# Performance work log

Measured on AMD Instinct MI355X. Metric: run time of the kernel, lower is better.

The kernel has to match this reference:

```python
import jax, jax.numpy as jnp
import numpy as np

B, S, D = 2, 2048, 2048
HQ, HK, HD = 16, 8, 128          # query heads, kv heads, head_dim
EPS = 1e-6
ROPE_THETA = 10000.0
SCALE = HD ** -0.5


def setup_inputs() -> dict:
    key = jax.random.key(0)
    ks = jax.random.split(key, 6)
    s = lambda fan_in: 1.0 / np.sqrt(fan_in)
    return {
        "hidden_states": jax.random.normal(ks[0], (B, S, D), jnp.float32),
        "positions": jnp.arange(S, dtype=jnp.int32),
        "Wq": jax.random.normal(ks[1], (D, HQ * HD), jnp.float32) * s(D),
        "Wk": jax.random.normal(ks[2], (D, HK * HD), jnp.float32) * s(D),
        "Wv": jax.random.normal(ks[3], (D, HK * HD), jnp.float32) * s(D),
        "Wo": jax.random.normal(ks[4], (HQ * HD, D), jnp.float32) * s(HQ * HD),
        "q_norm_w": jnp.ones((HD,), jnp.float32),
        "k_norm_w": jnp.ones((HD,), jnp.float32),
    }


def _rmsnorm(x, w):
    # RMSNorm over last (head_dim) axis, as in q_norm/k_norm
    var = jnp.mean(jnp.square(x), axis=-1, keepdims=True)
    return x * jax.lax.rsqrt(var + EPS) * w


def _rope(x, positions):
    # x: [B, S, H, HD]; rotate_half-style RoPE (Qwen3 convention)
    half = HD // 2
    inv_freq = 1.0 / (ROPE_THETA ** (jnp.arange(0, half, dtype=jnp.float32) / half))
    angles = positions.astype(jnp.float32)[:, None] * inv_freq[None, :]  # [S, half]
    cos = jnp.cos(angles)[None, :, None, :]  # [1, S, 1, half]
    sin = jnp.sin(angles)[None, :, None, :]
    x1, x2 = x[..., :half], x[..., half:]
    return jnp.concatenate([x1 * cos - x2 * sin, x2 * cos + x1 * sin], axis=-1)


def reference(hidden_states, positions, Wq, Wk, Wv, Wo, q_norm_w, k_norm_w):
    b, s, _ = hidden_states.shape
    q = (hidden_states @ Wq).reshape(b, s, HQ, HD)
    k = (hidden_states @ Wk).reshape(b, s, HK, HD)
    v = (hidden_states @ Wv).reshape(b, s, HK, HD)

    q = _rmsnorm(q, q_norm_w)
    k = _rmsnorm(k, k_norm_w)

    q = _rope(q, positions)
    k = _rope(k, positions)

    # GQA: repeat KV heads to match query heads
    groups = HQ // HK
    k = jnp.repeat(k, groups, axis=2)  # [B, S, HQ, HD]
    v = jnp.repeat(v, groups, axis=2)

    scores = jnp.einsum("bqhd,bkhd->bhqk", q, k) * SCALE  # [B, HQ, S, S]
    causal = jnp.tril(jnp.ones((s, s), dtype=bool))
    scores = jnp.where(causal[None, None], scores, jnp.float32(-jnp.inf))
    attn = jax.nn.softmax(scores, axis=-1)

    out = jnp.einsum("bhqk,bkhd->bqhd", attn, v).reshape(b, s, HQ * HD)
    return out @ Wo
```

## Files before the change

kernel.cpp:

```cpp
#include <hip/hip_runtime.h>
#include <cstdint>
#include <cstddef>

typedef _Float16 half8 __attribute__((ext_vector_type(8)));
typedef _Float16 half4 __attribute__((ext_vector_type(4)));
typedef float f32x4 __attribute__((ext_vector_type(4)));

#define DI __device__ __forceinline__

DI void gld_lds16(void* sp, const void* gp) {
  __builtin_amdgcn_global_load_lds(
      (const __attribute__((address_space(1))) void*)gp,
      (__attribute__((address_space(3))) void*)sp, 16, 0, 0);
}

template <int N>
DI void vmwait() { asm volatile("s_waitcnt vmcnt(%0)" :: "n"(N) : "memory"); }

DI void barrier_raw() {
  asm volatile("" ::: "memory");
  __builtin_amdgcn_s_barrier();
  asm volatile("" ::: "memory");
}

__global__ __launch_bounds__(256) void prep(const float* __restrict__ hs,
                                            const float* __restrict__ Wq,
                                            const float* __restrict__ Wk,
                                            const float* __restrict__ Wv,
                                            const float* __restrict__ Wo,
                                            _Float16* __restrict__ Xh,
                                            _Float16* __restrict__ Wqkvt,
                                            _Float16* __restrict__ Wot) {
  const int bid = blockIdx.x;
  if (bid >= 12288) {
    const int i = (bid - 12288) * 256 + threadIdx.x;
    const float4* p = (const float4*)hs + (size_t)i * 2;
    const float4 a = p[0], b = p[1];
    half8 h;
    h[0] = (_Float16)a.x; h[1] = (_Float16)a.y; h[2] = (_Float16)a.z; h[3] = (_Float16)a.w;
    h[4] = (_Float16)b.x; h[5] = (_Float16)b.y; h[6] = (_Float16)b.z; h[7] = (_Float16)b.w;
    *(half8*)(Xh + (size_t)i * 8) = h;
    return;
  }
  const float* in;
  _Float16* outp;
  int C, t;
  if (bid < 4096)      { in = Wq; outp = Wqkvt;                        C = 2048; t = bid; }
  else if (bid < 6144) { in = Wk; outp = Wqkvt + (size_t)2048 * 2048;  C = 1024; t = bid - 4096; }
  else if (bid < 8192) { in = Wv; outp = Wqkvt + (size_t)3072 * 2048;  C = 1024; t = bid - 6144; }
  else                 { in = Wo; outp = Wot;                          C = 2048; t = bid - 8192; }
  __shared__ float tl[32][33];
  const int tx = threadIdx.x & 31, ty = threadIdx.x >> 5;
  const int ctiles = C >> 5;
  const int tc = t % ctiles, tr = t / ctiles;
  const int r0 = tr * 32, c0 = tc * 32;
#pragma unroll
  for (int i = 0; i < 4; i++)
    tl[ty + 8 * i][tx] = in[(size_t)(r0 + ty + 8 * i) * C + c0 + tx];
  __syncthreads();
#pragma unroll
  for (int i = 0; i < 4; i++) {
    const int rr = ty + 8 * i;
    outp[(size_t)(c0 + rr) * 2048 + r0 + tx] = (_Float16)tl[tx][rr];
  }
}

#define QPHASE(Q, STAGE, VMW)                                                  \
  {                                                                            \
    half8 afr[2][2];                                                           \
    _Pragma("unroll") for (int j = 0; j < 2; j++)                              \
      _Pragma("unroll") for (int ks = 0; ks < 2; ks++) {                       \
        const int arow = wm * 128 + ((Q) * 2 + j) * 16 + lo;                   \
        afr[j][ks] =                                                           \
            *(const half8*)&sA[sa][arow * 64 + (((ks * 4 + hi) ^ lo7) << 3)];  \
      }                                                                        \
    STAGE;                                                                     \
    VMW;                                                                       \
    barrier_raw();                                                             \
    asm volatile("s_waitcnt lgkmcnt(0)" ::: "memory");                         \
    __builtin_amdgcn_sched_barrier(0);                                         \
    __builtin_amdgcn_s_setprio(1);                                             \
    _Pragma("unroll") for (int j = 0; j < 2; j++)                              \
      _Pragma("unroll") for (int nf = 0; nf < 4; nf++)                         \
        _Pragma("unroll") for (int ks = 0; ks < 2; ks++)                       \
          acc[(Q) * 2 + j][nf] = __builtin_amdgcn_mfma_f32_16x16x32_f16(       \
              afr[j][ks], bfr[nf][ks], acc[(Q) * 2 + j][nf], 0, 0, 0);         \
    __builtin_amdgcn_s_setprio(0);                                             \
    barrier_raw();                                                             \
  }

__global__ __launch_bounds__(512, 2) void gemm256(const _Float16* __restrict__ A,
                                                  const _Float16* __restrict__ Bt,
                                                  float* __restrict__ C,
                                                  int M, int N, int K) {
  __shared__ _Float16 sA[3][16384];
  __shared__ _Float16 sB[2][16384];
  const int tid = threadIdx.x, w = tid >> 6, l = tid & 63, lo = l & 15, hi = l >> 4;
  const int lo7 = lo & 7;
  const int wm = w >> 2, wn = w & 3;
  const int nbn = N >> 8;
  const int nwg = gridDim.x;
  int bid = blockIdx.x;
  bid = (bid & 7) * (nwg >> 3) + (bid >> 3);
  const int bm0 = (bid / nbn) << 8, bn0 = (bid % nbn) << 8;
  const int cswz = ((tid & 7) ^ ((tid >> 3) & 7)) << 3;
  const int NT = K >> 6;

  auto stageA = [&](int kt, int slot, int i0) {
#pragma unroll
    for (int ii = 0; ii < 2; ++ii) {
      const int i = i0 + ii;
      gld_lds16(&sA[slot][i * 4096 + (w << 9)],
                A + (size_t)(bm0 + i * 64 + (tid >> 3)) * K + kt * 64 + cswz);
    }
  };
  auto stageB = [&](int kt, int slot, int i0) {
#pragma unroll
    for (int ii = 0; ii < 2; ++ii) {
      const int i = i0 + ii;
      gld_lds16(&sB[slot][i * 4096 + (w << 9)],
                Bt + (size_t)(bn0 + i * 64 + (tid >> 3)) * K + kt * 64 + cswz);
    }
  };

  f32x4 acc[8][4];
#pragma unroll
  for (int mf = 0; mf < 8; mf++)
#pragma unroll
    for (int nf = 0; nf < 4; nf++)
#pragma unroll
      for (int r = 0; r < 4; r++) acc[mf][nf][r] = 0.0f;

  stageA(0, 0, 0); stageA(0, 0, 2);
  stageA(1, 1, 0); stageA(1, 1, 2);
  stageB(0, 0, 0); stageB(0, 0, 2);
  vmwait<0>();
  barrier_raw();

  int sa = 0, sa2 = 2;
#pragma unroll 1
  for (int t = 0; t < NT; ++t) {
    const int sb = t & 1, sb1 = sb ^ 1;
    half8 bfr[4][2];
#pragma unroll
    for (int nf = 0; nf < 4; nf++)
#pragma unroll
      for (int ks = 0; ks < 2; ks++) {
        const int brow = wn * 64 + nf * 16 + lo;
        bfr[nf][ks] = *(const half8*)&sB[sb][brow * 64 + (((ks * 4 + hi) ^ lo7) << 3)];
      }
    QPHASE(0, if (t + 1 < NT) stageB(t + 1, sb1, 0), )
    QPHASE(1, if (t + 1 < NT) stageB(t + 1, sb1, 2), )
    QPHASE(2, if (t + 2 < NT) stageA(t + 2, sa2, 0), )
    QPHASE(3, if (t + 2 < NT) stageA(t + 2, sa2, 2),
           if (t + 2 < NT) { vmwait<4>(); } else { vmwait<0>(); })
    sa = (sa == 2) ? 0 : sa + 1;
    sa2 = (sa2 == 2) ? 0 : sa2 + 1;
  }

#pragma unroll
  for (int mf = 0; mf < 8; mf++)
#pragma unroll
    for (int nf = 0; nf < 4; nf++)
#pragma unroll
      for (int r = 0; r < 4; r++)
        C[(size_t)(bm0 + wm * 128 + mf * 16 + hi * 4 + r) * N +
          (bn0 + wn * 64 + nf * 16 + lo)] = acc[mf][nf][r];
}

template <int BM, bool F16OUT>
__global__ __launch_bounds__(256) void gemm_bt(const _Float16* __restrict__ A,
                                               const _Float16* __restrict__ Bt,
                                               void* __restrict__ Cv,
                                               int M, int N, int K) {
  constexpr int MF = BM / 32;
  constexpr int LA = BM / 64;
  __shared__ _Float16 sA[2][BM * 32];
  __shared__ _Float16 sB[2][128 * 32];
  const int tid = threadIdx.x;
  const int w = tid >> 6, l = tid & 63, lo = l & 15, hi = l >> 4;
  const int gx = gridDim.x, nwg = gx * gridDim.y;
  int bid = blockIdx.y * gx + blockIdx.x;
  bid = (bid & 7) * (nwg >> 3) + (bid >> 3);
  const int bn0 = (bid % gx) * 128, bm0 = (bid / gx) * BM;
  const int wm = w >> 1, wn = w & 1;
  const int srow = l >> 2;
  const int csel = ((l & 3) ^ ((l >> 3) & 3)) * 8;
  const int kswz = (hi ^ ((lo >> 1) & 3)) * 8;

  f32x4 acc[MF][4];
#pragma unroll
  for (int mi = 0; mi < MF; mi++)
#pragma unroll
    for (int ni = 0; ni < 4; ni++)
#pragma unroll
      for (int r = 0; r < 4; r++) acc[mi][ni][r] = 0.0f;

  auto stage = [&](int bi, int kt) {
#pragma unroll
    for (int i = 0; i < LA; ++i) {
      const int j = LA * w + i;
      gld_lds16(&sA[bi][j * 512],
                A + (size_t)(bm0 + j * 16 + srow) * K + (size_t)kt * 32 + csel);
    }
#pragma unroll
    for (int i = 0; i < 2; ++i) {
      const int j = 2 * w + i;
      gld_lds16(&sB[bi][j * 512],
                Bt + (size_t)(bn0 + j * 16 + srow) * K + (size_t)kt * 32 + csel);
    }
  };

  stage(0, 0);
  __syncthreads();
  const int KT = K >> 5;
#pragma unroll 1
  for (int kt = 0; kt < KT; ++kt) {
    const int cur = kt & 1;
    if (kt + 1 < KT) stage(cur ^ 1, kt + 1);
    half8 a[MF], b[4];
#pragma unroll
    for (int mi = 0; mi < MF; mi++)
      a[mi] = *(const half8*)&sA[cur][(wm * (BM / 2) + mi * 16 + lo) * 32 + kswz];
#pragma unroll
    for (int ni = 0; ni < 4; ni++)
      b[ni] = *(const half8*)&sB[cur][(wn * 64 + ni * 16 + lo) * 32 + kswz];
#pragma unroll
    for (int mi = 0; mi < MF; mi++)
#pragma unroll
      for (int ni = 0; ni < 4; ni++)
        acc[mi][ni] = __builtin_amdgcn_mfma_f32_16x16x32_f16(a[mi], b[ni], acc[mi][ni], 0, 0, 0);
    __syncthreads();
  }

#pragma unroll
  for (int mi = 0; mi < MF; mi++)
#pragma unroll
    for (int ni = 0; ni < 4; ni++)
#pragma unroll
      for (int r = 0; r < 4; r++) {
        const size_t idx = (size_t)(bm0 + wm * (BM / 2) + mi * 16 + hi * 4 + r) * N +
                           (bn0 + wn * 64 + ni * 16 + lo);
        if constexpr (F16OUT) ((_Float16*)Cv)[idx] = (_Float16)acc[mi][ni][r];
        else                  ((float*)Cv)[idx] = acc[mi][ni][r];
      }
}

__global__ __launch_bounds__(256) void post(const float* __restrict__ QKV,
                                            const int* __restrict__ pos,
                                            const float* __restrict__ qw,
                                            const float* __restrict__ kw,
                                            _Float16* __restrict__ Qb,
                                            _Float16* __restrict__ Kb,
                                            _Float16* __restrict__ Vt) {
  if (blockIdx.x >= 24576) {
    __shared__ float tt[32][33];
    const int g = blockIdx.x - 24576;
    const int tx = threadIdx.x & 31, ty = threadIdx.x >> 5;
    const int dt = g & 3;
    const int st = (g >> 2) & 63;
    const int bh = g >> 8;
    const float* src = QKV + (size_t)((bh >> 3) * 2048 + st * 32) * 4096 +
                       3072 + (bh & 7) * 128 + dt * 32;
#pragma unroll
    for (int i = 0; i < 4; i++)
      tt[ty + 8 * i][tx] = src[(size_t)(ty + 8 * i) * 4096 + tx];
    __syncthreads();
    _Float16* dst = Vt + ((size_t)bh * 128 + dt * 32) * 2048 + st * 32;
#pragma unroll
    for (int i = 0; i < 4; i++) {
      const int rr = ty + 8 * i;
      dst[(size_t)rr * 2048 + tx] = (_Float16)tt[tx][rr];
    }
    return;
  }
  const int w = threadIdx.x >> 6, l = threadIdx.x & 63;
  const int wv = blockIdx.x * 4 + w;
  const int t = wv / 24, hh = wv - t * 24;
  const int b = t >> 11, s = t & 2047;
  const bool isq = hh < 16;
  const int col = isq ? hh * 128 : 2048 + (hh - 16) * 128;
  const float* x = QKV + (size_t)t * 4096 + col;
  const float x1 = x[l], x2 = x[l + 64];
  float ss = x1 * x1 + x2 * x2;
  ss += __shfl_xor(ss, 32); ss += __shfl_xor(ss, 16); ss += __shfl_xor(ss, 8);
  ss += __shfl_xor(ss, 4);  ss += __shfl_xor(ss, 2);  ss += __shfl_xor(ss, 1);
  const float rn = rsqrtf(ss * 0.0078125f + 1e-6f);
  const float* wt = isq ? qw : kw;
  const float n1 = x1 * rn * wt[l], n2 = x2 * rn * wt[l + 64];
  const float ang = (float)pos[s] * exp2f((float)l * -0.2076205059304601f);
  float sa, ca;
  sincosf(ang, &sa, &ca);
  const float qs = isq ? 0.12751731f : 1.0f;
  const float o1 = (n1 * ca - n2 * sa) * qs;
  const float o2 = (n2 * ca + n1 * sa) * qs;
  _Float16* dst = isq ? Qb + (((size_t)b * 16 + hh) * 2048 + s) * 128
                      : Kb + (((size_t)b * 8 + (hh - 16)) * 2048 + s) * 128;
  dst[l] = (_Float16)o1;
  dst[l + 64] = (_Float16)o2;
}

__global__ __launch_bounds__(256) void attn_fwd(const _Float16* __restrict__ Q,
                                                const _Float16* __restrict__ K,
                                                const _Float16* __restrict__ Vt,
                                                _Float16* __restrict__ AO) {
  __shared__ _Float16 sK[2][64 * 128];
  __shared__ _Float16 sV[2][128 * 64];
  __shared__ _Float16 P[4][16 * 80];
  const int tid = threadIdx.x, w = tid >> 6, l = tid & 63, lo = l & 15, hi = l >> 4;
  const int qt = 31 - (blockIdx.x >> 5);
  const int hq = blockIdx.x & 15;
  const int b = (blockIdx.x >> 4) & 1;
  const int hk = hq >> 1, q0 = qt * 64;
  const _Float16* Qh = Q + ((size_t)(b * 16 + hq) * 2048) * 128;
  const _Float16* Kh = K + ((size_t)(b * 8 + hk) * 2048) * 128;
  const _Float16* Vh = Vt + ((size_t)(b * 8 + hk) * 128) * 2048;
  const int qw0 = q0 + w * 16;

  auto stageK = [&](int bi, int kv0) {
#pragma unroll
    for (int i = 0; i < 4; ++i) {
      const int inst = w * 4 + i;
      const int r = inst * 4 + (l >> 4);
      const int cb = ((l & 15) * 16) ^ ((r & 7) << 4);
      gld_lds16(&sK[bi][inst * 512],
                (const char*)Kh + (size_t)(kv0 + r) * 256 + cb);
    }
  };
  auto stageV = [&](int bi, int kv0) {
#pragma unroll
    for (int i = 0; i < 4; ++i) {
      const int inst = w * 4 + i;
      const int r = inst * 8 + (l >> 3);
      const int cb = ((l & 7) * 16) ^ ((r & 7) << 4);
      gld_lds16(&sV[bi][inst * 512],
                (const char*)Vh + (size_t)r * 4096 + (size_t)kv0 * 2 + cb);
    }
  };

  half8 aq[4];
#pragma unroll
  for (int kc = 0; kc < 4; kc++)
    aq[kc] = *(const half8*)(Qh + (size_t)(qw0 + lo) * 128 + kc * 32 + hi * 8);

  f32x4 o[8];
#pragma unroll
  for (int dn = 0; dn < 8; dn++)
#pragma unroll
    for (int r = 0; r < 4; r++) o[dn][r] = 0.0f;
  float mrow = -1e30f, lrow = 0.0f;

  const int nt = qt + 1;
  stageK(0, 0);
  stageV(0, 0);
  __syncthreads();
#pragma unroll 1
  for (int kt = 0; kt < nt; ++kt) {
    const int kv0 = kt * 64;
    const int cur = kt & 1;
    if (kt + 1 < nt) {
      stageK(cur ^ 1, kv0 + 64);
      stageV(cur ^ 1, kv0 + 64);
    }
    const char* kb = (const char*)sK[cur];
    const char* vb = (const char*)sV[cur];
    f32x4 s[4];
#pragma unroll
    for (int ns = 0; ns < 4; ns++) {
#pragma unroll
      for (int r = 0; r < 4; r++) s[ns][r] = 0.0f;
      const int krow = ns * 16 + lo;
#pragma unroll
      for (int kc = 0; kc < 4; kc++) {
        half8 bk = *(const half8*)(kb + krow * 256 +
                                   ((kc * 64 + hi * 16) ^ ((krow & 7) << 4)));
        s[ns] = __builtin_amdgcn_mfma_f32_16x16x32_f16(bk, aq[kc], s[ns], 0, 0, 0);
      }
    }
    if (kt == nt - 1) {
#pragma unroll
      for (int ns = 0; ns < 4; ns++) {
        const int kv = kv0 + ns * 16 + hi * 4;
#pragma unroll
        for (int r = 0; r < 4; r++)
          if (kv + r > qw0 + lo) s[ns][r] = -1e30f;
      }
    }
    float tmax = s[0][0];
#pragma unroll
    for (int ns = 0; ns < 4; ns++)
#pragma unroll
      for (int r = 0; r < 4; r++) tmax = fmaxf(tmax, s[ns][r]);
    tmax = fmaxf(tmax, __shfl_xor(tmax, 16));
    tmax = fmaxf(tmax, __shfl_xor(tmax, 32));
    if (!__all(tmax <= mrow + 8.0f)) {
      const float mn = fmaxf(mrow, tmax);
      const float corr = exp2f(mrow - mn);
      mrow = mn;
      lrow *= corr;
      float c4[4];
#pragma unroll
      for (int r = 0; r < 4; r++) c4[r] = __shfl(corr, hi * 4 + r, 16);
#pragma unroll
      for (int dn = 0; dn < 8; dn++)
#pragma unroll
        for (int r = 0; r < 4; r++) o[dn][r] *= c4[r];
    }
    float psum = 0.0f;
#pragma unroll
    for (int ns = 0; ns < 4; ns++) {
      half4 pk;
#pragma unroll
      for (int r = 0; r < 4; r++) {
        const float p = exp2f(s[ns][r] - mrow);
        psum += p;
        pk[r] = (_Float16)p;
      }
      *(half4*)&P[w][lo * 80 + ns * 16 + hi * 4] = pk;
    }
    psum += __shfl_xor(psum, 16);
    psum += __shfl_xor(psum, 32);
    lrow += psum;
    asm volatile("s_waitcnt lgkmcnt(0)" ::: "memory");
    half8 ap0 = *(const half8*)&P[w][lo * 80 + hi * 8];
    half8 ap1 = *(const half8*)&P[w][lo * 80 + 32 + hi * 8];
#pragma unroll
    for (int dn = 0; dn < 8; dn++) {
      const int vrow = dn * 16 + lo;
      half8 bv0 = *(const half8*)(vb + vrow * 128 + ((hi * 16) ^ ((vrow & 7) << 4)));
      half8 bv1 = *(const half8*)(vb + vrow * 128 + ((64 + hi * 16) ^ ((vrow & 7) << 4)));
      o[dn] = __builtin_amdgcn_mfma_f32_16x16x32_f16(ap0, bv0, o[dn], 0, 0, 0);
      o[dn] = __builtin_amdgcn_mfma_f32_16x16x32_f16(ap1, bv1, o[dn], 0, 0, 0);
    }
    __syncthreads();
  }

  const float inv = 1.0f / lrow;
  float i4[4];
#pragma unroll
  for (int r = 0; r < 4; r++) i4[r] = __shfl(inv, hi * 4 + r, 16);
  const size_t tok = (size_t)b * 2048 + qw0;
#pragma unroll
  for (int dn = 0; dn < 8; dn++)
#pragma unroll
    for (int r = 0; r < 4; r++)
      AO[(tok + hi * 4 + r) * 2048 + hq * 128 + dn * 16 + lo] = (_Float16)(o[dn][r] * i4[r]);
}

extern "C" void kernel_launch(void* const* d_in, const int* in_sizes, int n_in,
                              void* d_out, int out_size, void* d_ws, size_t ws_size,
                              hipStream_t stream) {
  (void)in_sizes; (void)n_in; (void)out_size; (void)ws_size;
  const float* hs  = (const float*)d_in[0];
  const int*   pos = (const int*)d_in[1];
  const float* Wq  = (const float*)d_in[2];
  const float* Wk  = (const float*)d_in[3];
  const float* Wv  = (const float*)d_in[4];
  const float* Wo  = (const float*)d_in[5];
  const float* qnw = (const float*)d_in[6];
  const float* knw = (const float*)d_in[7];
  float* out = (float*)d_out;

  char* ws = (char*)d_ws;
  size_t off = 0;
  auto take = [&](size_t bytes) -> void* {
    void* p = ws + off;
    off += (bytes + 255) & ~(size_t)255;
    return p;
  };
  _Float16* Xh    = (_Float16*)take((size_t)4096 * 2048 * 2);
  _Float16* Wqkvt = (_Float16*)take((size_t)4096 * 2048 * 2);
  _Float16* Wot   = (_Float16*)take((size_t)2048 * 2048 * 2);
  float*    QKV   = (float*)take((size_t)4096 * 4096 * 4);
  _Float16* Qb    = (_Float16*)take((size_t)2 * 16 * 2048 * 128 * 2);
  _Float16* Kb    = (_Float16*)take((size_t)2 * 8 * 2048 * 128 * 2);
  _Float16* Vt    = (_Float16*)take((size_t)2 * 8 * 128 * 2048 * 2);
  _Float16* AO    = (_Float16*)take((size_t)4096 * 2048 * 2);

  prep<<<16384, 256, 0, stream>>>(hs, Wq, Wk, Wv, Wo, Xh, Wqkvt, Wot);
  gemm256<<<256, 512, 0, stream>>>(Xh, Wqkvt, QKV, 4096, 4096, 2048);
  post<<<28672, 256, 0, stream>>>(QKV, pos, qnw, knw, Qb, Kb, Vt);
  attn_fwd<<<1024, 256, 0, stream>>>(Qb, Kb, Vt, AO);
  gemm_bt<64, false><<<dim3(16, 64), 256, 0, stream>>>(AO, Wot, out, 4096, 2048, 2048);
}
```

Before: 236.1 us.

## Load V fragments directly from global into registers, drop V LDS staging

Removes the double-buffered shared-memory staging of the transposed V tile and instead has each wave load its V MFMA operands straight from global memory into registers at the top of each KV iteration. It also sets launch_bounds to 256 threads with a minimum of 3 blocks per CU. The intent is to cut LDS footprint and LDS traffic so more blocks fit per CU. In exchange, every wave issues redundant global loads of the same V tile, which relies on the cache, and the 16 half8 registers per thread raise register pressure, with possible spills under the 3-block bound.

```diff
diff --git a/kernel.cpp b/kernel.cpp
--- a/kernel.cpp
+++ b/kernel.cpp
@@ -300,12 +300,11 @@
   dst[l + 64] = (_Float16)o2;
 }
 
-__global__ __launch_bounds__(256) void attn_fwd(const _Float16* __restrict__ Q,
-                                                const _Float16* __restrict__ K,
-                                                const _Float16* __restrict__ Vt,
-                                                _Float16* __restrict__ AO) {
+__global__ __launch_bounds__(256, 3) void attn_fwd(const _Float16* __restrict__ Q,
+                                                   const _Float16* __restrict__ K,
+                                                   const _Float16* __restrict__ Vt,
+                                                   _Float16* __restrict__ AO) {
   __shared__ _Float16 sK[2][64 * 128];
-  __shared__ _Float16 sV[2][128 * 64];
   __shared__ _Float16 P[4][16 * 80];
   const int tid = threadIdx.x, w = tid >> 6, l = tid & 63, lo = l & 15, hi = l >> 4;
   const int qt = 31 - (blockIdx.x >> 5);
@@ -327,16 +326,6 @@
                 (const char*)Kh + (size_t)(kv0 + r) * 256 + cb);
     }
   };
-  auto stageV = [&](int bi, int kv0) {
-#pragma unroll
-    for (int i = 0; i < 4; ++i) {
-      const int inst = w * 4 + i;
-      const int r = inst * 8 + (l >> 3);
-      const int cb = ((l & 7) * 16) ^ ((r & 7) << 4);
-      gld_lds16(&sV[bi][inst * 512],
-                (const char*)Vh + (size_t)r * 4096 + (size_t)kv0 * 2 + cb);
-    }
-  };
 
   half8 aq[4];
 #pragma unroll
@@ -352,18 +341,20 @@
 
   const int nt = qt + 1;
   stageK(0, 0);
-  stageV(0, 0);
   __syncthreads();
 #pragma unroll 1
   for (int kt = 0; kt < nt; ++kt) {
     const int kv0 = kt * 64;
     const int cur = kt & 1;
-    if (kt + 1 < nt) {
-      stageK(cur ^ 1, kv0 + 64);
-      stageV(cur ^ 1, kv0 + 64);
-    }
+    half8 bv[8][2];
+#pragma unroll
+    for (int dn = 0; dn < 8; dn++) {
+      const _Float16* vp = Vh + (size_t)(dn * 16 + lo) * 2048 + kv0 + hi * 8;
+      bv[dn][0] = *(const half8*)vp;
+      bv[dn][1] = *(const half8*)(vp + 32);
+    }
+    if (kt + 1 < nt) stageK(cur ^ 1, kv0 + 64);
     const char* kb = (const char*)sK[cur];
-    const char* vb = (const char*)sV[cur];
     f32x4 s[4];
 #pragma unroll
     for (int ns = 0; ns < 4; ns++) {
@@ -426,11 +417,8 @@
     half8 ap1 = *(const half8*)&P[w][lo * 80 + 32 + hi * 8];
 #pragma unroll
     for (int dn = 0; dn < 8; dn++) {
-      const int vrow = dn * 16 + lo;
-      half8 bv0 = *(const half8*)(vb + vrow * 128 + ((hi * 16) ^ ((vrow & 7) << 4)));
-      half8 bv1 = *(const half8*)(vb + vrow * 128 + ((64 + hi * 16) ^ ((vrow & 7) << 4)));
-      o[dn] = __builtin_amdgcn_mfma_f32_16x16x32_f16(ap0, bv0, o[dn], 0, 0, 0);
-      o[dn] = __builtin_amdgcn_mfma_f32_16x16x32_f16(ap1, bv1, o[dn], 0, 0, 0);
+      o[dn] = __builtin_amdgcn_mfma_f32_16x16x32_f16(ap0, bv[dn][0], o[dn], 0, 0, 0);
+      o[dn] = __builtin_amdgcn_mfma_f32_16x16x32_f16(ap1, bv[dn][1], o[dn], 0, 0, 0);
     }
     __syncthreads();
   }
```

Measured after the change: 305.5 us. 1.29x slower.
